# Optimization experiments

Measured on AMD Instinct MI355X. Metric: run time of the kernel, lower is better.

The kernel has to match this reference:

```python
import jax, jax.numpy as jnp
import numpy as np

V, D, L, H, FF, MAXLEN, M = 128, 512, 4, 8, 2048, 1024, 4
B, T = 2, 1024
DK = D // H
EPS = 1e-5  # F.layer_norm default


def setup_inputs() -> dict:
    key = jax.random.key(0)
    ks = jax.random.split(key, 10)
    x = jax.random.randint(ks[0], (B, T), 0, V)
    inp = {
        'x': x,
        'tok_emb': 0.02 * jax.random.normal(ks[1], (M, V, D), jnp.float32),
        'pos_emb': 0.02 * jax.random.normal(ks[2], (M, MAXLEN, D), jnp.float32),
        'ln1_w': jnp.ones((L, M, D), jnp.float32),
        'ln1_b': jnp.zeros((L, M, D), jnp.float32),
        'qkv_w': jax.random.normal(ks[3], (L, M, 3 * D, D), jnp.float32) * (1.0 / np.sqrt(D)),
        'qkv_b': jnp.zeros((L, M, 3 * D), jnp.float32),
        'out_w': jax.random.normal(ks[4], (L, M, D, D), jnp.float32) * (1.0 / np.sqrt(D)),
        'out_b': jnp.zeros((L, M, D), jnp.float32),
        'ln2_w': jnp.ones((L, M, D), jnp.float32),
        'ln2_b': jnp.zeros((L, M, D), jnp.float32),
        'ff1_w': jax.random.normal(ks[5], (L, M, FF, D), jnp.float32) * (1.0 / np.sqrt(D)),
        'ff1_b': jnp.zeros((L, M, FF), jnp.float32),
        'ff2_w': jax.random.normal(ks[6], (L, M, D, FF), jnp.float32) * (1.0 / np.sqrt(FF)),
        'ff2_b': jnp.zeros((L, M, D), jnp.float32),
        'lnf_w': jnp.ones((M, D), jnp.float32),
        'lnf_b': jnp.zeros((M, D), jnp.float32),
        'head_w': jax.random.normal(ks[7], (M, V, D), jnp.float32) * (1.0 / np.sqrt(D)),
        'head_b': jnp.zeros((M, V), jnp.float32),
    }
    return inp


def _layernorm(h, w, b):
    # h: [M,B,T,D], w/b: [M,D]
    mu = h.mean(-1, keepdims=True)
    var = ((h - mu) ** 2).mean(-1, keepdims=True)
    return (h - mu) / jnp.sqrt(var + EPS) * w[:, None, None, :] + b[:, None, None, :]


def reference(x, tok_emb, pos_emb, ln1_w, ln1_b, qkv_w, qkv_b, out_w, out_b,
              ln2_w, ln2_b, ff1_w, ff1_b, ff2_w, ff2_b, lnf_w, lnf_b, head_w, head_b):
    Bx, Tx = x.shape
    # token + positional embedding, batched over the model axis -> [M,B,T,D]
    h = tok_emb[:, x] + pos_emb[:, None, :Tx, :]
    mask = jnp.tril(jnp.ones((Tx, Tx), bool))  # causal
    scale = 1.0 / np.sqrt(DK).astype(np.float32)
    for l in range(L):
        n = _layernorm(h, ln1_w[l], ln1_b[l])
        qkv = jnp.einsum('mbtd,mfd->mbtf', n, qkv_w[l]) + qkv_b[l][:, None, None, :]
        # (M,B,T,H,3*DK) -> (M,B,H,T,3*DK); chunk last dim into q,k,v (matches torch chunk)
        qkv = qkv.reshape(h.shape[0], Bx, Tx, H, 3 * DK).transpose(0, 1, 3, 2, 4)
        q, k, v = jnp.split(qkv, 3, axis=-1)
        s = jnp.einsum('mbhtd,mbhsd->mbhts', q, k) * scale
        s = jnp.where(mask, s, -jnp.inf)
        a = jax.nn.softmax(s, axis=-1)
        o = jnp.einsum('mbhts,mbhsd->mbhtd', a, v)
        o = o.transpose(0, 1, 3, 2, 4).reshape(h.shape[0], Bx, Tx, D)
        o = jnp.einsum('mbtd,med->mbte', o, out_w[l]) + out_b[l][:, None, None, :]
        h = h + o
        n = _layernorm(h, ln2_w[l], ln2_b[l])
        f = jax.nn.relu(jnp.einsum('mbtd,mfd->mbtf', n, ff1_w[l]) + ff1_b[l][:, None, None, :])
        f = jnp.einsum('mbtf,mdf->mbtd', f, ff2_w[l]) + ff2_b[l][:, None, None, :]
        h = h + f
    h = _layernorm(h, lnf_w, lnf_b)
    logits = jnp.einsum('mbtd,mvd->mbtv', h, head_w) + head_b[:, None, None, :]
    return logits.transpose(1, 0, 2, 3)  # (B, model_count, T, V) like torch.stack(dim=1)
```

## Files before the change

### kernel.cpp

```cpp
#include <hip/hip_runtime.h>

#define M_  4
#define B_  2
#define T_  1024
#define D_  512
#define V_  128
#define L_  4
#define H_  8
#define FF_ 2048
#define DK_ 64
#define BT_ (B_*T_)
#define EPS_ 1e-5f

typedef __attribute__((ext_vector_type(8))) short  bf16x8;
typedef __attribute__((ext_vector_type(4))) float  f32x4;
typedef __attribute__((ext_vector_type(8))) ushort ushort8v;

__device__ __forceinline__ float b2f(ushort u) {
  union { unsigned int i; float f; } c; c.i = ((unsigned int)u) << 16; return c.f;
}
__device__ __forceinline__ ushort f2b(float f) {
  union { float f; unsigned int i; } c; c.f = f;
  return (ushort)((c.i + 0x7FFFu + ((c.i >> 16) & 1u)) >> 16);
}
__device__ __forceinline__ void gload_lds16(const void* g, void* l) {
  __builtin_amdgcn_global_load_lds((const __attribute__((address_space(1))) unsigned int*)g,
                                   (__attribute__((address_space(3))) unsigned int*)l, 16, 0, 0);
}

__global__ __launch_bounds__(128)
void k_embed(const int* __restrict__ x, const float* __restrict__ tok,
             const float* __restrict__ pos, float* __restrict__ h)
{
  const int t = blockIdx.x, b = blockIdx.y, m = blockIdx.z;
  const int d = threadIdx.x * 4;
  const int xv = x[b*T_ + t];
  const float4 tv = *(const float4*)&tok[((size_t)m*V_ + xv)*D_ + d];
  const float4 pv = *(const float4*)&pos[((size_t)m*1024 + t)*D_ + d];
  float4 r;
  r.x = tv.x + pv.x; r.y = tv.y + pv.y; r.z = tv.z + pv.z; r.w = tv.w + pv.w;
  *(float4*)&h[(((size_t)m*B_ + b)*T_ + t)*D_ + d] = r;
}

#define NQ8_ 393216
#define NO8_ 131072
#define NF8_ 524288
__global__ __launch_bounds__(256)
void k_cvt4(const float* __restrict__ s0, const float* __restrict__ s1,
            const float* __restrict__ s2, const float* __restrict__ s3,
            ushort* __restrict__ d0, ushort* __restrict__ d1,
            ushort* __restrict__ d2, ushort* __restrict__ d3)
{
  int i = blockIdx.x * 256 + threadIdx.x;
  const float* s; ushort* d;
  if (i < NQ8_)                    { s = s0; d = d0; }
  else if (i < NQ8_+NO8_)          { s = s1; d = d1; i -= NQ8_; }
  else if (i < NQ8_+NO8_+NF8_)     { s = s2; d = d2; i -= NQ8_+NO8_; }
  else                             { s = s3; d = d3; i -= NQ8_+NO8_+NF8_; }
  const float4 a = ((const float4*)s)[i*2];
  const float4 b = ((const float4*)s)[i*2+1];
  ushort8v o;
  o[0]=f2b(a.x); o[1]=f2b(a.y); o[2]=f2b(a.z); o[3]=f2b(a.w);
  o[4]=f2b(b.x); o[5]=f2b(b.y); o[6]=f2b(b.z); o[7]=f2b(b.w);
  ((ushort8v*)d)[i] = o;
}

__global__ __launch_bounds__(256)
void k_cvt(const float* __restrict__ src, ushort* __restrict__ dst, int n8)
{
  const int i = blockIdx.x * 256 + threadIdx.x;
  if (i >= n8) return;
  const float4 a = ((const float4*)src)[i*2];
  const float4 b = ((const float4*)src)[i*2+1];
  ushort8v o;
  o[0]=f2b(a.x); o[1]=f2b(a.y); o[2]=f2b(a.z); o[3]=f2b(a.w);
  o[4]=f2b(b.x); o[5]=f2b(b.y); o[6]=f2b(b.z); o[7]=f2b(b.w);
  ((ushort8v*)dst)[i] = o;
}

__global__ __launch_bounds__(256)
void k_ln(const float* __restrict__ x, const float* __restrict__ w,
          const float* __restrict__ bb, ushort* __restrict__ y)
{
  const int row  = blockIdx.x * 4 + (threadIdx.x >> 6);
  const int lane = threadIdx.x & 63;
  const int m = row >> 11;
  const float* xp = x + (size_t)row*D_ + lane*8;
  const float4 v0 = *(const float4*)xp;
  const float4 v1 = *(const float4*)(xp + 4);
  float s  = v0.x+v0.y+v0.z+v0.w + v1.x+v1.y+v1.z+v1.w;
  float s2 = v0.x*v0.x+v0.y*v0.y+v0.z*v0.z+v0.w*v0.w
           + v1.x*v1.x+v1.y*v1.y+v1.z*v1.z+v1.w*v1.w;
  #pragma unroll
  for (int off = 1; off < 64; off <<= 1) {
    s  += __shfl_xor(s, off);
    s2 += __shfl_xor(s2, off);
  }
  const float mu   = s * (1.0f/D_);
  const float var  = s2 * (1.0f/D_) - mu*mu;
  const float rstd = rsqrtf(var + EPS_);
  const float* wp = w + m*D_ + lane*8;
  const float* bp = bb + m*D_ + lane*8;
  const float4 w0 = *(const float4*)wp, w1 = *(const float4*)(wp+4);
  const float4 b0 = *(const float4*)bp, b1 = *(const float4*)(bp+4);
  ushort8v o;
  o[0]=f2b((v0.x-mu)*rstd*w0.x+b0.x); o[1]=f2b((v0.y-mu)*rstd*w0.y+b0.y);
  o[2]=f2b((v0.z-mu)*rstd*w0.z+b0.z); o[3]=f2b((v0.w-mu)*rstd*w0.w+b0.w);
  o[4]=f2b((v1.x-mu)*rstd*w1.x+b1.x); o[5]=f2b((v1.y-mu)*rstd*w1.y+b1.y);
  o[6]=f2b((v1.z-mu)*rstd*w1.z+b1.z); o[7]=f2b((v1.w-mu)*rstd*w1.w+b1.w);
  *(ushort8v*)&y[(size_t)row*D_ + lane*8] = o;
}

template<int OUTBF, int ACT, int RES, int HEADOUT, int SPLITV>
__global__ __launch_bounds__(256)
void k_gemm(const ushort* __restrict__ A, const ushort* __restrict__ W,
            const float* __restrict__ bias, const float* __restrict__ resid,
            void* __restrict__ C, ushort* __restrict__ vt, int RR, int NN, int KK)
{
  const int m  = blockIdx.z;
  const int r0 = blockIdx.x * 128;
  const int c0 = blockIdx.y * 128;
  const ushort* Am = A + (size_t)m*RR*KK;
  const ushort* Wm = W + (size_t)m*NN*KK;

  __shared__ ushort As[2][128*64];
  __shared__ ushort Bs[2][128*64];

  const int tid  = threadIdx.x;
  const int lane = tid & 63;
  const int wave = tid >> 6;
  const int wr = wave >> 1, wc = wave & 1;
  const int fr = lane & 15;
  const int fq = lane >> 4;

  f32x4 acc[4][4];
  #pragma unroll
  for (int i = 0; i < 4; ++i)
    #pragma unroll
    for (int j = 0; j < 4; ++j)
      acc[i][j] = (f32x4){0.f,0.f,0.f,0.f};

  #pragma unroll
  for (int i = 0; i < 4; ++i) {
    const int c = i*256 + tid;
    const int row = c >> 3, ch = c & 7;
    const int sch = ch ^ (row & 7);
    gload_lds16(Am + (size_t)(r0+row)*KK + sch*8, (ushort*)As[0] + (size_t)c*8);
    gload_lds16(Wm + (size_t)(c0+row)*KK + sch*8, (ushort*)Bs[0] + (size_t)c*8);
  }
  __syncthreads();

  const int NK = KK >> 6;
  for (int kt = 0; kt < NK; ++kt) {
    const int cur = kt & 1;

    if (kt + 1 < NK) {
      const int k0 = (kt + 1) * 64;
      #pragma unroll
      for (int i = 0; i < 4; ++i) {
        const int c = i*256 + tid;
        const int row = c >> 3, ch = c & 7;
        const int sch = ch ^ (row & 7);
        gload_lds16(Am + (size_t)(r0+row)*KK + k0 + sch*8, (ushort*)As[cur^1] + (size_t)c*8);
        gload_lds16(Wm + (size_t)(c0+row)*KK + k0 + sch*8, (ushort*)Bs[cur^1] + (size_t)c*8);
      }
      asm volatile("s_waitcnt vmcnt(8)" ::: "memory");
    } else {
      asm volatile("s_waitcnt vmcnt(0)" ::: "memory");
    }
    __builtin_amdgcn_sched_barrier(0);
    __builtin_amdgcn_s_barrier();

    #pragma unroll
    for (int kk = 0; kk < 2; ++kk) {
      bf16x8 af[4], bfv[4];
      #pragma unroll
      for (int i = 0; i < 4; ++i) {
        const int rowA = wr*64 + i*16 + fr;
        af[i]  = *(const bf16x8*)&As[cur][rowA*64 + (((kk*4 + fq) ^ (rowA & 7))*8)];
        const int rowB = wc*64 + i*16 + fr;
        bfv[i] = *(const bf16x8*)&Bs[cur][rowB*64 + (((kk*4 + fq) ^ (rowB & 7))*8)];
      }
      #pragma unroll
      for (int i = 0; i < 4; ++i)
        #pragma unroll
        for (int j = 0; j < 4; ++j)
          acc[i][j] = __builtin_amdgcn_mfma_f32_16x16x32_bf16(af[i], bfv[j], acc[i][j], 0, 0, 0);
    }
    __builtin_amdgcn_s_barrier();
  }

  const int colb = c0 + wc*64 + fr;
  float bi[4];
  #pragma unroll
  for (int j = 0; j < 4; ++j) bi[j] = bias[(size_t)m*NN + colb + j*16];

  if (SPLITV) {
    #pragma unroll
    for (int i = 0; i < 4; ++i) {
      const int row0 = r0 + wr*64 + i*16 + fq*4;
      const int mbg = (blockIdx.z)*B_ + (row0 >> 10);
      const int t0  = row0 & 1023;
      #pragma unroll
      for (int j = 0; j < 4; ++j) {
        const int col = colb + j*16;
        const int hh2 = col / 192;
        const int sub = col - hh2*192;
        float v0 = acc[i][j][0] + bi[j];
        float v1 = acc[i][j][1] + bi[j];
        float v2 = acc[i][j][2] + bi[j];
        float v3 = acc[i][j][3] + bi[j];
        if (sub >= 128) {
          ushort4 pk;
          pk.x = f2b(v0); pk.y = f2b(v1); pk.z = f2b(v2); pk.w = f2b(v3);
          *(ushort4*)&vt[(((size_t)mbg*8 + hh2)*64 + (sub-128))*1024 + t0] = pk;
        } else {
          ushort* cp = (ushort*)C + ((size_t)m*RR + row0)*NN + col;
          cp[0*NN] = f2b(v0); cp[1*NN] = f2b(v1); cp[2*NN] = f2b(v2); cp[3*NN] = f2b(v3);
        }
      }
    }
  } else {
    #pragma unroll
    for (int i = 0; i < 4; ++i) {
      #pragma unroll
      for (int r = 0; r < 4; ++r) {
        const int row = r0 + wr*64 + i*16 + fq*4 + r;
        #pragma unroll
        for (int j = 0; j < 4; ++j) {
          float val = acc[i][j][r] + bi[j];
          if (ACT) val = fmaxf(val, 0.0f);
          const int col = colb + j*16;
          size_t oidx;
          if (HEADOUT) {
            const int b = row >> 10, t = row & 1023;
            oidx = (((size_t)b*M_ + m)*T_ + t)*V_ + col;
          } else {
            oidx = ((size_t)m*RR + row)*NN + col;
          }
          float v2 = val;
          if (RES) v2 += resid[oidx];
          if (OUTBF) ((ushort*)C)[oidx] = f2b(v2);
          else       ((float*)C)[oidx]  = v2;
        }
      }
    }
  }
}

__global__ __launch_bounds__(256)
void k_attn_mfma(const ushort* __restrict__ qkvb, const ushort* __restrict__ vt,
                 ushort* __restrict__ o)
{
  const int pair = blockIdx.x;
  const int hh   = blockIdx.y;
  const int mbg  = blockIdx.z;

  __shared__ ushort Qs[64*64];
  __shared__ ushort Ks[2][64*64];
  __shared__ ushort Vs[2][64*64];
  __shared__ ushort Ps[4][16*80];

  const int tid  = threadIdx.x;
  const int lane = tid & 63;
  const int wave = tid >> 6;
  const int fr = lane & 15;
  const int fq = lane >> 4;

  const ushort* qk_base = qkvb + (size_t)mbg*T_*(3*D_) + hh*(3*DK_);
  const ushort* vt_base = vt + ((size_t)(mbg*8 + hh)*64)*1024;
  const float SCALE2 = 0.125f * 1.44269504f;

  #pragma unroll 1
  for (int pass = 0; pass < 2; ++pass) {
    const int qb = pass ? (15 - pair) : pair;

    #pragma unroll
    for (int i = 0; i < 2; ++i) {
      const int c = wave*128 + i*64 + lane;
      const int row = c >> 3, ch = c & 7;
      const int sch = (ch ^ (row & 7)) * 8;
      gload_lds16(qk_base + (size_t)(qb*64 + row)*(3*D_) + sch,
                  (ushort*)Qs + (size_t)(wave*128 + i*64)*8);
      gload_lds16(qk_base + (size_t)row*(3*D_) + DK_ + sch,
                  (ushort*)Ks[0] + (size_t)(wave*128 + i*64)*8);
      gload_lds16(vt_base + (size_t)row*1024 + sch,
                  (ushort*)Vs[0] + (size_t)(wave*128 + i*64)*8);
    }
    __syncthreads();

    bf16x8 aQ[2];
    #pragma unroll
    for (int kc = 0; kc < 2; ++kc) {
      const int qrow = wave*16 + fr;
      aQ[kc] = *(const bf16x8*)&Qs[qrow*64 + (((kc*4 + fq) ^ (qrow&7))*8)];
    }

    float m_q = -3.0e38f, l_q = 0.0f;
    f32x4 Of[4];
    #pragma unroll
    for (int j = 0; j < 4; ++j) Of[j] = (f32x4){0.f,0.f,0.f,0.f};

    const int qrow_abs0 = qb*64 + wave*16 + fq*4;

    auto tile = [&](int kb, bool DIAG, bool PRE) {
      const int cur = kb & 1;
      if (PRE) {
        #pragma unroll
        for (int i = 0; i < 2; ++i) {
          const int c = wave*128 + i*64 + lane;
          const int row = c >> 3, ch = c & 7;
          const int sch = (ch ^ (row & 7)) * 8;
          gload_lds16(qk_base + (size_t)((kb+1)*64 + row)*(3*D_) + DK_ + sch,
                      (ushort*)Ks[cur^1] + (size_t)(wave*128 + i*64)*8);
          gload_lds16(vt_base + (size_t)row*1024 + (kb+1)*64 + sch,
                      (ushort*)Vs[cur^1] + (size_t)(wave*128 + i*64)*8);
        }
        asm volatile("s_waitcnt vmcnt(4)" ::: "memory");
      } else {
        asm volatile("s_waitcnt vmcnt(0)" ::: "memory");
      }
      __builtin_amdgcn_sched_barrier(0);
      __builtin_amdgcn_s_barrier();

      f32x4 acc[4];
      #pragma unroll
      for (int j = 0; j < 4; ++j) acc[j] = (f32x4){0.f,0.f,0.f,0.f};
      __builtin_amdgcn_s_setprio(1);
      #pragma unroll
      for (int kc = 0; kc < 2; ++kc) {
        #pragma unroll
        for (int j = 0; j < 4; ++j) {
          const int krow = j*16 + fr;
          const bf16x8 bK = *(const bf16x8*)&Ks[cur][krow*64 + (((kc*4 + fq) ^ (krow&7))*8)];
          acc[j] = __builtin_amdgcn_mfma_f32_16x16x32_bf16(bK, aQ[kc], acc[j], 0, 0, 0);
        }
      }
      __builtin_amdgcn_s_setprio(0);

      float sv[16];
      float rm = -3.0e38f;
      #pragma unroll
      for (int j = 0; j < 4; ++j)
        #pragma unroll
        for (int r = 0; r < 4; ++r) {
          float v = acc[j][r] * SCALE2;
          if (DIAG && (j*16 + fq*4 + r) > (wave*16 + fr)) v = -3.0e38f;
          sv[j*4+r] = v;
          rm = fmaxf(rm, v);
        }
      rm = fmaxf(rm, __shfl_xor(rm, 16));
      rm = fmaxf(rm, __shfl_xor(rm, 32));
      if (!__all(rm - m_q <= 8.0f)) {
        const float mn = fmaxf(m_q, rm);
        const float sc = exp2f(m_q - mn);
        m_q = mn;
        l_q *= sc;
        float scr[4];
        #pragma unroll
        for (int r = 0; r < 4; ++r) scr[r] = __shfl(sc, fq*4 + r);
        #pragma unroll
        for (int j = 0; j < 4; ++j)
          #pragma unroll
          for (int r = 0; r < 4; ++r) Of[j][r] *= scr[r];
      }
      float p[16], rs = 0.0f;
      #pragma unroll
      for (int i2 = 0; i2 < 16; ++i2) {
        p[i2] = exp2f(sv[i2] - m_q);
        rs += p[i2];
      }
      rs += __shfl_xor(rs, 16);
      rs += __shfl_xor(rs, 32);
      l_q += rs;

      #pragma unroll
      for (int j = 0; j < 4; ++j) {
        unsigned int lo, hi;
        asm("v_cvt_pk_bf16_f32 %0, %1, %2" : "=v"(lo) : "v"(p[j*4+0]), "v"(p[j*4+1]));
        asm("v_cvt_pk_bf16_f32 %0, %1, %2" : "=v"(hi) : "v"(p[j*4+2]), "v"(p[j*4+3]));
        const int idx = (fr*80 + j*16 + fq*4) ^ ((fr>>2)<<4);
        *(unsigned int*)&Ps[wave][idx]     = lo;
        *(unsigned int*)&Ps[wave][idx + 2] = hi;
      }

      __builtin_amdgcn_s_setprio(1);
      #pragma unroll
      for (int kc = 0; kc < 2; ++kc) {
        const int pidx = fr*80 + kc*32 + fq*8;
        const bf16x8 pa = *(const bf16x8*)&Ps[wave][pidx ^ ((fr>>2)<<4)];
        #pragma unroll
        for (int j = 0; j < 4; ++j) {
          const int vrow = j*16 + fr;
          const bf16x8 bV = *(const bf16x8*)&Vs[cur][vrow*64 + (((kc*4 + fq) ^ (vrow&7))*8)];
          Of[j] = __builtin_amdgcn_mfma_f32_16x16x32_bf16(pa, bV, Of[j], 0, 0, 0);
        }
      }
      __builtin_amdgcn_s_setprio(0);
      __builtin_amdgcn_s_barrier();
    };

    for (int kb = 0; kb < qb; ++kb) tile(kb, false, true);
    tile(qb, true, false);

    const float linv = 1.0f / l_q;
    float inv[4];
    #pragma unroll
    for (int r = 0; r < 4; ++r) inv[r] = __shfl(linv, fq*4 + r);
    #pragma unroll
    for (int r = 0; r < 4; ++r) {
      ushort* op = o + ((size_t)mbg*T_ + (qrow_abs0 + r))*D_ + hh*DK_ + fr;
      #pragma unroll
      for (int j = 0; j < 4; ++j)
        op[j*16] = f2b(Of[j][r] * inv[r]);
    }
  }
}

extern "C" void kernel_launch(void* const* d_in, const int* in_sizes, int n_in,
                              void* d_out, int out_size, void* d_ws, size_t ws_size,
                              hipStream_t stream)
{
  const int*   x       = (const int*)  d_in[0];
  const float* tok_emb = (const float*)d_in[1];
  const float* pos_emb = (const float*)d_in[2];
  const float* ln1_w   = (const float*)d_in[3];
  const float* ln1_b   = (const float*)d_in[4];
  const float* qkv_w   = (const float*)d_in[5];
  const float* qkv_b   = (const float*)d_in[6];
  const float* out_w   = (const float*)d_in[7];
  const float* out_b   = (const float*)d_in[8];
  const float* ln2_w   = (const float*)d_in[9];
  const float* ln2_b   = (const float*)d_in[10];
  const float* ff1_w   = (const float*)d_in[11];
  const float* ff1_b   = (const float*)d_in[12];
  const float* ff2_w   = (const float*)d_in[13];
  const float* ff2_b   = (const float*)d_in[14];
  const float* lnf_w   = (const float*)d_in[15];
  const float* lnf_b   = (const float*)d_in[16];
  const float* head_w  = (const float*)d_in[17];
  const float* head_b  = (const float*)d_in[18];
  float* outp = (float*)d_out;

  const size_t HS = (size_t)M_*B_*T_*D_;
  float*  h     = (float*)d_ws;
  ushort* nb    = (ushort*)(h + HS);
  ushort* qkvb  = nb + HS;
  ushort* ob    = qkvb + (size_t)M_*B_*T_*3*D_;
  ushort* fb    = qkvb;
  ushort* vtb   = ob + HS;
  ushort* wq    = vtb + HS;
  ushort* wo    = wq  + (size_t)M_*3*D_*D_;
  ushort* wf1   = wo  + (size_t)M_*D_*D_;
  ushort* wf2   = wf1 + (size_t)M_*FF_*D_;

  const int ROWS = M_*B_*T_;
  const int NH = M_*V_*D_/8;
  const int CVT4_BLK = (NQ8_ + NO8_ + NF8_ + NF8_) / 256;

  k_embed<<<dim3(T_, B_, M_), 128, 0, stream>>>(x, tok_emb, pos_emb, h);

  for (int l = 0; l < L_; ++l) {
    k_cvt4<<<CVT4_BLK, 256, 0, stream>>>(
        qkv_w + (size_t)l*M_*3*D_*D_, out_w + (size_t)l*M_*D_*D_,
        ff1_w + (size_t)l*M_*FF_*D_,  ff2_w + (size_t)l*M_*D_*FF_,
        wq, wo, wf1, wf2);

    k_ln<<<ROWS/4, 256, 0, stream>>>(h, ln1_w + l*M_*D_, ln1_b + l*M_*D_, nb);

    k_gemm<1,0,0,0,1><<<dim3(BT_/128, (3*D_)/128, M_), 256, 0, stream>>>(
        nb, wq, qkv_b + l*M_*3*D_, nullptr, qkvb, vtb, BT_, 3*D_, D_);

    k_attn_mfma<<<dim3(T_/128, H_, M_*B_), 256, 0, stream>>>(qkvb, vtb, ob);

    k_gemm<0,0,1,0,0><<<dim3(BT_/128, D_/128, M_), 256, 0, stream>>>(
        ob, wo, out_b + l*M_*D_, h, h, nullptr, BT_, D_, D_);

    k_ln<<<ROWS/4, 256, 0, stream>>>(h, ln2_w + l*M_*D_, ln2_b + l*M_*D_, nb);

    k_gemm<1,1,0,0,0><<<dim3(BT_/128, FF_/128, M_), 256, 0, stream>>>(
        nb, wf1, ff1_b + l*M_*FF_, nullptr, fb, nullptr, BT_, FF_, D_);

    k_gemm<0,0,1,0,0><<<dim3(BT_/128, D_/128, M_), 256, 0, stream>>>(
        fb, wf2, ff2_b + l*M_*D_, h, h, nullptr, BT_, D_, FF_);
  }

  k_ln<<<ROWS/4, 256, 0, stream>>>(h, lnf_w, lnf_b, nb);
  k_cvt<<<NH/256, 256, 0, stream>>>(head_w, wq, NH);
  k_gemm<0,0,0,1,0><<<dim3(BT_/128, V_/128, M_), 256, 0, stream>>>(
      nb, wq, head_b, nullptr, outp, nullptr, BT_, V_, D_);
}
```

Measured before the change: 598.9 us.

## Convert all weights in one launch and split attention into one query-block per workgroup

All four layers' weights and the head weights are now converted to bf16 in a single kernel at the start, written into per-layer slabs. This replaces five separate conversion launches but needs a much larger workspace. The attention kernel no longer loops over two paired query blocks per workgroup. It launches one workgroup per query block, interleaved so heavy and light causal blocks alternate, which doubles the grid to raise parallelism. The GEMM prologue also drops a __syncthreads and relies on the wait and barrier inside the main loop.

New measurement: 749.6 us. 1.25x slower.

```diff
diff --git a/kernel.cpp b/kernel.cpp
--- a/kernel.cpp
+++ b/kernel.cpp
@@ -45,37 +45,33 @@
 #define NQ8_ 393216
 #define NO8_ 131072
 #define NF8_ 524288
+#define LSLAB_ 12582912
 __global__ __launch_bounds__(256)
-void k_cvt4(const float* __restrict__ s0, const float* __restrict__ s1,
-            const float* __restrict__ s2, const float* __restrict__ s3,
-            ushort* __restrict__ d0, ushort* __restrict__ d1,
-            ushort* __restrict__ d2, ushort* __restrict__ d3)
-{
-  int i = blockIdx.x * 256 + threadIdx.x;
+void k_cvt_all(const float* __restrict__ qkv_w, const float* __restrict__ out_w,
+               const float* __restrict__ ff1_w, const float* __restrict__ ff2_w,
+               const float* __restrict__ head_w, ushort* __restrict__ wall)
+{
+  const int bx = blockIdx.x;
+  long i;
   const float* s; ushort* d;
-  if (i < NQ8_)                    { s = s0; d = d0; }
-  else if (i < NQ8_+NO8_)          { s = s1; d = d1; i -= NQ8_; }
-  else if (i < NQ8_+NO8_+NF8_)     { s = s2; d = d2; i -= NQ8_+NO8_; }
-  else                             { s = s3; d = d3; i -= NQ8_+NO8_+NF8_; }
+  if (bx < 4*6144) {
+    const int l = bx / 6144;
+    i = (long)(bx % 6144)*256 + threadIdx.x;
+    ushort* base = wall + (size_t)l*LSLAB_;
+    if (i < NQ8_)                    { s = qkv_w + (size_t)l*3145728; d = base; }
+    else if (i < NQ8_+NO8_)          { s = out_w + (size_t)l*1048576; d = base + 3145728; i -= NQ8_; }
+    else if (i < NQ8_+NO8_+NF8_)     { s = ff1_w + (size_t)l*4194304; d = base + 4194304; i -= NQ8_+NO8_; }
+    else                             { s = ff2_w + (size_t)l*4194304; d = base + 8388608; i -= NQ8_+NO8_+NF8_; }
+  } else {
+    i = (long)(bx - 4*6144)*256 + threadIdx.x;
+    s = head_w; d = wall + (size_t)4*LSLAB_;
+  }
   const float4 a = ((const float4*)s)[i*2];
   const float4 b = ((const float4*)s)[i*2+1];
   ushort8v o;
   o[0]=f2b(a.x); o[1]=f2b(a.y); o[2]=f2b(a.z); o[3]=f2b(a.w);
   o[4]=f2b(b.x); o[5]=f2b(b.y); o[6]=f2b(b.z); o[7]=f2b(b.w);
   ((ushort8v*)d)[i] = o;
-}
-
-__global__ __launch_bounds__(256)
-void k_cvt(const float* __restrict__ src, ushort* __restrict__ dst, int n8)
-{
-  const int i = blockIdx.x * 256 + threadIdx.x;
-  if (i >= n8) return;
-  const float4 a = ((const float4*)src)[i*2];
-  const float4 b = ((const float4*)src)[i*2+1];
-  ushort8v o;
-  o[0]=f2b(a.x); o[1]=f2b(a.y); o[2]=f2b(a.z); o[3]=f2b(a.w);
-  o[4]=f2b(b.x); o[5]=f2b(b.y); o[6]=f2b(b.z); o[7]=f2b(b.w);
-  ((ushort8v*)dst)[i] = o;
 }
 
 __global__ __launch_bounds__(256)
@@ -148,7 +144,6 @@
     gload_lds16(Am + (size_t)(r0+row)*KK + sch*8, (ushort*)As[0] + (size_t)c*8);
     gload_lds16(Wm + (size_t)(c0+row)*KK + sch*8, (ushort*)Bs[0] + (size_t)c*8);
   }
-  __syncthreads();
 
   const int NK = KK >> 6;
   for (int kt = 0; kt < NK; ++kt) {
@@ -252,7 +247,8 @@
 void k_attn_mfma(const ushort* __restrict__ qkvb, const ushort* __restrict__ vt,
                  ushort* __restrict__ o)
 {
-  const int pair = blockIdx.x;
+  const int xb   = blockIdx.x;
+  const int qb   = (xb & 1) ? (15 - (xb >> 1)) : (xb >> 1);
   const int hh   = blockIdx.y;
   const int mbg  = blockIdx.z;
 
@@ -271,149 +267,144 @@
   const ushort* vt_base = vt + ((size_t)(mbg*8 + hh)*64)*1024;
   const float SCALE2 = 0.125f * 1.44269504f;
 
-  #pragma unroll 1
-  for (int pass = 0; pass < 2; ++pass) {
-    const int qb = pass ? (15 - pair) : pair;
-
-    #pragma unroll
-    for (int i = 0; i < 2; ++i) {
-      const int c = wave*128 + i*64 + lane;
-      const int row = c >> 3, ch = c & 7;
-      const int sch = (ch ^ (row & 7)) * 8;
-      gload_lds16(qk_base + (size_t)(qb*64 + row)*(3*D_) + sch,
-                  (ushort*)Qs + (size_t)(wave*128 + i*64)*8);
-      gload_lds16(qk_base + (size_t)row*(3*D_) + DK_ + sch,
-                  (ushort*)Ks[0] + (size_t)(wave*128 + i*64)*8);
-      gload_lds16(vt_base + (size_t)row*1024 + sch,
-                  (ushort*)Vs[0] + (size_t)(wave*128 + i*64)*8);
-    }
-    __syncthreads();
-
-    bf16x8 aQ[2];
+  #pragma unroll
+  for (int i = 0; i < 2; ++i) {
+    const int c = wave*128 + i*64 + lane;
+    const int row = c >> 3, ch = c & 7;
+    const int sch = (ch ^ (row & 7)) * 8;
+    gload_lds16(qk_base + (size_t)(qb*64 + row)*(3*D_) + sch,
+                (ushort*)Qs + (size_t)(wave*128 + i*64)*8);
+    gload_lds16(qk_base + (size_t)row*(3*D_) + DK_ + sch,
+                (ushort*)Ks[0] + (size_t)(wave*128 + i*64)*8);
+    gload_lds16(vt_base + (size_t)row*1024 + sch,
+                (ushort*)Vs[0] + (size_t)(wave*128 + i*64)*8);
+  }
+  __syncthreads();
+
+  bf16x8 aQ[2];
+  #pragma unroll
+  for (int kc = 0; kc < 2; ++kc) {
+    const int qrow = wave*16 + fr;
+    aQ[kc] = *(const bf16x8*)&Qs[qrow*64 + (((kc*4 + fq) ^ (qrow&7))*8)];
+  }
+
+  float m_q = -3.0e38f, l_q = 0.0f;
+  f32x4 Of[4];
+  #pragma unroll
+  for (int j = 0; j < 4; ++j) Of[j] = (f32x4){0.f,0.f,0.f,0.f};
+
+  const int qrow_abs0 = qb*64 + wave*16 + fq*4;
+
+  auto tile = [&](int kb, bool DIAG, bool PRE) {
+    const int cur = kb & 1;
+    if (PRE) {
+      #pragma unroll
+      for (int i = 0; i < 2; ++i) {
+        const int c = wave*128 + i*64 + lane;
+        const int row = c >> 3, ch = c & 7;
+        const int sch = (ch ^ (row & 7)) * 8;
+        gload_lds16(qk_base + (size_t)((kb+1)*64 + row)*(3*D_) + DK_ + sch,
+                    (ushort*)Ks[cur^1] + (size_t)(wave*128 + i*64)*8);
+        gload_lds16(vt_base + (size_t)row*1024 + (kb+1)*64 + sch,
+                    (ushort*)Vs[cur^1] + (size_t)(wave*128 + i*64)*8);
+      }
+      asm volatile("s_waitcnt vmcnt(4)" ::: "memory");
+    } else {
+      asm volatile("s_waitcnt vmcnt(0)" ::: "memory");
+    }
+    __builtin_amdgcn_sched_barrier(0);
+    __builtin_amdgcn_s_barrier();
+
+    f32x4 acc[4];
+    #pragma unroll
+    for (int j = 0; j < 4; ++j) acc[j] = (f32x4){0.f,0.f,0.f,0.f};
+    __builtin_amdgcn_s_setprio(1);
     #pragma unroll
     for (int kc = 0; kc < 2; ++kc) {
-      const int qrow = wave*16 + fr;
-      aQ[kc] = *(const bf16x8*)&Qs[qrow*64 + (((kc*4 + fq) ^ (qrow&7))*8)];
-    }
-
-    float m_q = -3.0e38f, l_q = 0.0f;
-    f32x4 Of[4];
-    #pragma unroll
-    for (int j = 0; j < 4; ++j) Of[j] = (f32x4){0.f,0.f,0.f,0.f};
-
-    const int qrow_abs0 = qb*64 + wave*16 + fq*4;
-
-    auto tile = [&](int kb, bool DIAG, bool PRE) {
-      const int cur = kb & 1;
-      if (PRE) {
-        #pragma unroll
-        for (int i = 0; i < 2; ++i) {
-          const int c = wave*128 + i*64 + lane;
-          const int row = c >> 3, ch = c & 7;
-          const int sch = (ch ^ (row & 7)) * 8;
-          gload_lds16(qk_base + (size_t)((kb+1)*64 + row)*(3*D_) + DK_ + sch,
-                      (ushort*)Ks[cur^1] + (size_t)(wave*128 + i*64)*8);
-          gload_lds16(vt_base + (size_t)row*1024 + (kb+1)*64 + sch,
-                      (ushort*)Vs[cur^1] + (size_t)(wave*128 + i*64)*8);
-        }
-        asm volatile("s_waitcnt vmcnt(4)" ::: "memory");
-      } else {
-        asm volatile("s_waitcnt vmcnt(0)" ::: "memory");
-      }
-      __builtin_amdgcn_sched_barrier(0);
-      __builtin_amdgcn_s_barrier();
-
-      f32x4 acc[4];
-      #pragma unroll
-      for (int j = 0; j < 4; ++j) acc[j] = (f32x4){0.f,0.f,0.f,0.f};
-      __builtin_amdgcn_s_setprio(1);
-      #pragma unroll
-      for (int kc = 0; kc < 2; ++kc) {
-        #pragma unroll
-        for (int j = 0; j < 4; ++j) {
-          const int krow = j*16 + fr;
-          const bf16x8 bK = *(const bf16x8*)&Ks[cur][krow*64 + (((kc*4 + fq) ^ (krow&7))*8)];
-          acc[j] = __builtin_amdgcn_mfma_f32_16x16x32_bf16(bK, aQ[kc], acc[j], 0, 0, 0);
-        }
-      }
-      __builtin_amdgcn_s_setprio(0);
-
-      float sv[16];
-      float rm = -3.0e38f;
+      #pragma unroll
+      for (int j = 0; j < 4; ++j) {
+        const int krow = j*16 + fr;
+        const bf16x8 bK = *(const bf16x8*)&Ks[cur][krow*64 + (((kc*4 + fq) ^ (krow&7))*8)];
+        acc[j] = __builtin_amdgcn_mfma_f32_16x16x32_bf16(bK, aQ[kc], acc[j], 0, 0, 0);
+      }
+    }
+    __builtin_amdgcn_s_setprio(0);
+
+    float sv[16];
+    float rm = -3.0e38f;
+    #pragma unroll
+    for (int j = 0; j < 4; ++j)
+      #pragma unroll
+      for (int r = 0; r < 4; ++r) {
+        float v = acc[j][r] * SCALE2;
+        if (DIAG && (j*16 + fq*4 + r) > (wave*16 + fr)) v = -3.0e38f;
+        sv[j*4+r] = v;
+        rm = fmaxf(rm, v);
+      }
+    rm = fmaxf(rm, __shfl_xor(rm, 16));
+    rm = fmaxf(rm, __shfl_xor(rm, 32));
+    if (!__all(rm - m_q <= 8.0f)) {
+      const float mn = fmaxf(m_q, rm);
+      const float sc = exp2f(m_q - mn);
+      m_q = mn;
+      l_q *= sc;
+      float scr[4];
+      #pragma unroll
+      for (int r = 0; r < 4; ++r) scr[r] = __shfl(sc, fq*4 + r);
       #pragma unroll
       for (int j = 0; j < 4; ++j)
         #pragma unroll
-        for (int r = 0; r < 4; ++r) {
-          float v = acc[j][r] * SCALE2;
-          if (DIAG && (j*16 + fq*4 + r) > (wave*16 + fr)) v = -3.0e38f;
-          sv[j*4+r] = v;
-          rm = fmaxf(rm, v);
-        }
-      rm = fmaxf(rm, __shfl_xor(rm, 16));
-      rm = fmaxf(rm, __shfl_xor(rm, 32));
-      if (!__all(rm - m_q <= 8.0f)) {
-        const float mn = fmaxf(m_q, rm);
-        const float sc = exp2f(m_q - mn);
-        m_q = mn;
-        l_q *= sc;
-        float scr[4];
-        #pragma unroll
-        for (int r = 0; r < 4; ++r) scr[r] = __shfl(sc, fq*4 + r);
-        #pragma unroll
-        for (int j = 0; j < 4; ++j)
-          #pragma unroll
-          for (int r = 0; r < 4; ++r) Of[j][r] *= scr[r];
-      }
-      float p[16], rs = 0.0f;
-      #pragma unroll
-      for (int i2 = 0; i2 < 16; ++i2) {
-        p[i2] = exp2f(sv[i2] - m_q);
-        rs += p[i2];
-      }
-      rs += __shfl_xor(rs, 16);
-      rs += __shfl_xor(rs, 32);
-      l_q += rs;
-
+        for (int r = 0; r < 4; ++r) Of[j][r] *= scr[r];
+    }
+    float p[16], rs = 0.0f;
+    #pragma unroll
+    for (int i2 = 0; i2 < 16; ++i2) {
+      p[i2] = exp2f(sv[i2] - m_q);
+      rs += p[i2];
+    }
+    rs += __shfl_xor(rs, 16);
+    rs += __shfl_xor(rs, 32);
+    l_q += rs;
+
+    #pragma unroll
+    for (int j = 0; j < 4; ++j) {
+      unsigned int lo, hi;
+      asm("v_cvt_pk_bf16_f32 %0, %1, %2" : "=v"(lo) : "v"(p[j*4+0]), "v"(p[j*4+1]));
+      asm("v_cvt_pk_bf16_f32 %0, %1, %2" : "=v"(hi) : "v"(p[j*4+2]), "v"(p[j*4+3]));
+      const int idx = (fr*80 + j*16 + fq*4) ^ ((fr>>2)<<4);
+      *(unsigned int*)&Ps[wave][idx]     = lo;
+      *(unsigned int*)&Ps[wave][idx + 2] = hi;
+    }
+
+    __builtin_amdgcn_s_setprio(1);
+    #pragma unroll
+    for (int kc = 0; kc < 2; ++kc) {
+      const int pidx = fr*80 + kc*32 + fq*8;
+      const bf16x8 pa = *(const bf16x8*)&Ps[wave][pidx ^ ((fr>>2)<<4)];
       #pragma unroll
       for (int j = 0; j < 4; ++j) {
-        unsigned int lo, hi;
-        asm("v_cvt_pk_bf16_f32 %0, %1, %2" : "=v"(lo) : "v"(p[j*4+0]), "v"(p[j*4+1]));
-        asm("v_cvt_pk_bf16_f32 %0, %1, %2" : "=v"(hi) : "v"(p[j*4+2]), "v"(p[j*4+3]));
-        const int idx = (fr*80 + j*16 + fq*4) ^ ((fr>>2)<<4);
-        *(unsigned int*)&Ps[wave][idx]     = lo;
-        *(unsigned int*)&Ps[wave][idx + 2] = hi;
-      }
-
-      __builtin_amdgcn_s_setprio(1);
-      #pragma unroll
-      for (int kc = 0; kc < 2; ++kc) {
-        const int pidx = fr*80 + kc*32 + fq*8;
-        const bf16x8 pa = *(const bf16x8*)&Ps[wave][pidx ^ ((fr>>2)<<4)];
-        #pragma unroll
-        for (int j = 0; j < 4; ++j) {
-          const int vrow = j*16 + fr;
-          const bf16x8 bV = *(const bf16x8*)&Vs[cur][vrow*64 + (((kc*4 + fq) ^ (vrow&7))*8)];
-          Of[j] = __builtin_amdgcn_mfma_f32_16x16x32_bf16(pa, bV, Of[j], 0, 0, 0);
-        }
-      }
-      __builtin_amdgcn_s_setprio(0);
-      __builtin_amdgcn_s_barrier();
-    };
-
-    for (int kb = 0; kb < qb; ++kb) tile(kb, false, true);
-    tile(qb, true, false);
-
-    const float linv = 1.0f / l_q;
-    float inv[4];
-    #pragma unroll
-    for (int r = 0; r < 4; ++r) inv[r] = __shfl(linv, fq*4 + r);
-    #pragma unroll
-    for (int r = 0; r < 4; ++r) {
-      ushort* op = o + ((size_t)mbg*T_ + (qrow_abs0 + r))*D_ + hh*DK_ + fr;
-      #pragma unroll
-      for (int j = 0; j < 4; ++j)
-        op[j*16] = f2b(Of[j][r] * inv[r]);
-    }
+        const int vrow = j*16 + fr;
+        const bf16x8 bV = *(const bf16x8*)&Vs[cur][vrow*64 + (((kc*4 + fq) ^ (vrow&7))*8)];
+        Of[j] = __builtin_amdgcn_mfma_f32_16x16x32_bf16(pa, bV, Of[j], 0, 0, 0);
+      }
+    }
+    __builtin_amdgcn_s_setprio(0);
+    __builtin_amdgcn_s_barrier();
+  };
+
+  for (int kb = 0; kb < qb; ++kb) tile(kb, false, true);
+  tile(qb, true, false);
+
+  const float linv = 1.0f / l_q;
+  float inv[4];
+  #pragma unroll
+  for (int r = 0; r < 4; ++r) inv[r] = __shfl(linv, fq*4 + r);
+  #pragma unroll
+  for (int r = 0; r < 4; ++r) {
+    ushort* op = o + ((size_t)mbg*T_ + (qrow_abs0 + r))*D_ + hh*DK_ + fr;
+    #pragma unroll
+    for (int j = 0; j < 4; ++j)
+      op[j*16] = f2b(Of[j][r] * inv[r]);
   }
 }
 
@@ -449,29 +440,26 @@
   ushort* ob    = qkvb + (size_t)M_*B_*T_*3*D_;
   ushort* fb    = qkvb;
   ushort* vtb   = ob + HS;
-  ushort* wq    = vtb + HS;
-  ushort* wo    = wq  + (size_t)M_*3*D_*D_;
-  ushort* wf1   = wo  + (size_t)M_*D_*D_;
-  ushort* wf2   = wf1 + (size_t)M_*FF_*D_;
+  ushort* wall  = vtb + HS;
+  ushort* wh    = wall + (size_t)4*LSLAB_;
 
   const int ROWS = M_*B_*T_;
-  const int NH = M_*V_*D_/8;
-  const int CVT4_BLK = (NQ8_ + NO8_ + NF8_ + NF8_) / 256;
-
+
+  k_cvt_all<<<4*6144 + 128, 256, 0, stream>>>(qkv_w, out_w, ff1_w, ff2_w, head_w, wall);
   k_embed<<<dim3(T_, B_, M_), 128, 0, stream>>>(x, tok_emb, pos_emb, h);
 
   for (int l = 0; l < L_; ++l) {
-    k_cvt4<<<CVT4_BLK, 256, 0, stream>>>(
-        qkv_w + (size_t)l*M_*3*D_*D_, out_w + (size_t)l*M_*D_*D_,
-        ff1_w + (size_t)l*M_*FF_*D_,  ff2_w + (size_t)l*M_*D_*FF_,
-        wq, wo, wf1, wf2);
+    ushort* wq  = wall + (size_t)l*LSLAB_;
+    ushort* wo  = wq  + 3145728;
+    ushort* wf1 = wo  + 1048576;
+    ushort* wf2 = wf1 + 4194304;
 
     k_ln<<<ROWS/4, 256, 0, stream>>>(h, ln1_w + l*M_*D_, ln1_b + l*M_*D_, nb);
 
     k_gemm<1,0,0,0,1><<<dim3(BT_/128, (3*D_)/128, M_), 256, 0, stream>>>(
         nb, wq, qkv_b + l*M_*3*D_, nullptr, qkvb, vtb, BT_, 3*D_, D_);
 
-    k_attn_mfma<<<dim3(T_/128, H_, M_*B_), 256, 0, stream>>>(qkvb, vtb, ob);
+    k_attn_mfma<<<dim3(16, H_, M_*B_), 256, 0, stream>>>(qkvb, vtb, ob);
 
     k_gemm<0,0,1,0,0><<<dim3(BT_/128, D_/128, M_), 256, 0, stream>>>(
         ob, wo, out_b + l*M_*D_, h, h, nullptr, BT_, D_, D_);
@@ -486,7 +474,6 @@
   }
 
   k_ln<<<ROWS/4, 256, 0, stream>>>(h, lnf_w, lnf_b, nb);
-  k_cvt<<<NH/256, 256, 0, stream>>>(head_w, wq, NH);
   k_gemm<0,0,0,1,0><<<dim3(BT_/128, V_/128, M_), 256, 0, stream>>>(
-      nb, wq, head_b, nullptr, outp, nullptr, BT_, V_, D_);
-}
+      nb, wh, head_b, nullptr, outp, nullptr, BT_, V_, D_);
+}
```
